# Kernel optimization log

Hardware: AMD Instinct MI355X
Metric: run time of the kernel (lower is better)

## Reference

```python
import jax, jax.numpy as jnp
import numpy as np

LN_EPS = 1e-5


def setup_inputs() -> dict:
    key = jax.random.key(0)
    k1, k2, k3 = jax.random.split(key, 3)
    B, E, IN, OUT = 16384, 8, 1024, 1024
    w_bound = (6.0 / (IN * OUT)) ** 0.5
    x = jax.random.normal(k1, (B, IN), dtype=jnp.float32)
    coef = jax.random.uniform(k2, (B, E), dtype=jnp.float32)
    w = jax.random.uniform(k3, (E, OUT, IN), dtype=jnp.float32,
                           minval=-w_bound, maxval=w_bound)
    b = jnp.zeros((E, OUT), dtype=jnp.float32)
    gamma = jnp.ones((OUT,), dtype=jnp.float32)
    beta = jnp.zeros((OUT,), dtype=jnp.float32)
    return {"x": x, "coef": coef, "w": w, "b": b, "gamma": gamma, "beta": beta}


def reference(x, coef, w, b, gamma, beta):
    # Soft-MoE linear: algebraically identical to the torch einsum chain
    #   w_b = einsum('be,ejk->bjk'); y = einsum('bk,bjk->bj') + einsum('be,ek->bk')
    # Reordered to avoid materializing [B,out,in]:
    #   per-expert projections [B,E,out], then coef-weighted combine.
    y = jnp.einsum('bk,ejk->bej', x, w)          # [B, E, out]
    y = jnp.einsum('be,bej->bj', coef, y)        # [B, out]
    y = y + coef @ b                              # [B, out]
    # LayerNorm(out_channels)
    mu = jnp.mean(y, axis=-1, keepdims=True)
    var = jnp.mean(jnp.square(y - mu), axis=-1, keepdims=True)
    y = (y - mu) * jax.lax.rsqrt(var + LN_EPS) * gamma + beta
    # GELU (torch nn.GELU default = exact erf form)
    y = jax.nn.gelu(y, approximate=False)
    return y
```

## Files before the change

### kernel.cpp

```cpp
#include <hip/hip_runtime.h>
#include <hip/hip_bf16.h>


typedef __attribute__((ext_vector_type(8))) short bf16x8;
typedef __attribute__((ext_vector_type(4))) float f32x4;

__device__ __forceinline__ unsigned short f2bf_rn(float f) {
    union { float f; unsigned u; } v; v.f = f;
    unsigned r = v.u + 0x7FFFu + ((v.u >> 16) & 1u);
    return (unsigned short)(r >> 16);
}
__device__ __forceinline__ float bf2f(unsigned short h) {
    union { unsigned u; float f; } v; v.u = ((unsigned)h) << 16; return v.f;
}

__global__ __launch_bounds__(256) void split_f32_bf16(
        const float* __restrict__ in, unsigned short* __restrict__ hi,
        unsigned short* __restrict__ lo, int n4) {
    int i = blockIdx.x * blockDim.x + threadIdx.x;
    const int stride = gridDim.x * blockDim.x;
    for (; i < n4; i += stride) {
        float4 v = ((const float4*)in)[i];
        ushort4 h, l;
        h.x = f2bf_rn(v.x); l.x = f2bf_rn(v.x - bf2f(h.x));
        h.y = f2bf_rn(v.y); l.y = f2bf_rn(v.y - bf2f(h.y));
        h.z = f2bf_rn(v.z); l.z = f2bf_rn(v.z - bf2f(h.z));
        h.w = f2bf_rn(v.w); l.w = f2bf_rn(v.w - bf2f(h.w));
        ((ushort4*)hi)[i] = h;
        ((ushort4*)lo)[i] = l;
    }
}

#define BM 256
#define BN 128
#define BK 32
#define NT 512

#define GLD(gp, lp) __builtin_amdgcn_global_load_lds( \
    (const __attribute__((address_space(1))) void*)(gp), \
    (__attribute__((address_space(3))) void*)(lp), 16, 0, 0)

__global__ __launch_bounds__(NT, 2) void gemm_moe(
        const unsigned short* __restrict__ xh, const unsigned short* __restrict__ xl,
        const unsigned short* __restrict__ wh, const unsigned short* __restrict__ wl,
        const float* __restrict__ coef, float* __restrict__ y) {
    __shared__ unsigned short As_h[BM * BK];
    __shared__ unsigned short As_l[BM * BK];
    __shared__ unsigned short Bs_h[BN * BK];
    __shared__ unsigned short Bs_l[BN * BK];

    const int bid = blockIdx.x;
    const int nb = bid & 7;
    const int mb = bid >> 3;
    const int m0 = mb * BM, n0 = nb * BN;
    const int t = threadIdx.x;
    const int lane = t & 63;
    const int wid = t >> 6;
    const int wm = wid >> 1, wn = wid & 1;
    const int lr = lane & 15, kg = lane >> 4;

    const int ar = t >> 2;
    const int acs = (t & 3) ^ (ar & 3);
    const unsigned short* agh = xh + (size_t)(m0 + ar) * 1024 + acs * 8;
    const unsigned short* agl = xl + (size_t)(m0 + ar) * 1024 + acs * 8;
    const int br = t >> 2;
    const int bcs = (t & 3) ^ (br & 3);
    const size_t bofs = (size_t)(n0 + br) * 1024 + bcs * 8;

    int aoff[4], boff[4];
#pragma unroll
    for (int i = 0; i < 4; ++i) {
        int row = wm * 64 + i * 16 + lr;
        aoff[i] = row * BK + ((kg ^ (lr & 3)) * 8);
    }
#pragma unroll
    for (int j = 0; j < 4; ++j) {
        int row = wn * 64 + j * 16 + lr;
        boff[j] = row * BK + ((kg ^ (lr & 3)) * 8);
    }

    f32x4 acc_t[4][4] = {};

    for (int e = 0; e < 8; ++e) {
        f32x4 acc[4][4] = {};
        const unsigned short* wh_e = wh + (size_t)e * 1048576 + bofs;
        const unsigned short* wl_e = wl + (size_t)e * 1048576 + bofs;
#pragma unroll 1
        for (int kt = 0; kt < 1024 / BK; ++kt) {
            const int k = kt * BK;
            __syncthreads();
            GLD(agh + k,          As_h + t * 8);
            GLD(agh + 131072 + k, As_h + 4096 + t * 8);
            GLD(agl + k,          As_l + t * 8);
            GLD(agl + 131072 + k, As_l + 4096 + t * 8);
            GLD(wh_e + k,         Bs_h + t * 8);
            GLD(wl_e + k,         Bs_l + t * 8);
            __syncthreads();

            bf16x8 ah[4], al[4], bh[4], bl[4];
#pragma unroll
            for (int i = 0; i < 4; ++i) {
                ah[i] = *(const bf16x8*)(As_h + aoff[i]);
                al[i] = *(const bf16x8*)(As_l + aoff[i]);
            }
#pragma unroll
            for (int j = 0; j < 4; ++j) {
                bh[j] = *(const bf16x8*)(Bs_h + boff[j]);
                bl[j] = *(const bf16x8*)(Bs_l + boff[j]);
            }
#pragma unroll
            for (int i = 0; i < 4; ++i)
#pragma unroll
                for (int j = 0; j < 4; ++j) {
                    acc[i][j] = __builtin_amdgcn_mfma_f32_16x16x32_bf16(
                        ah[i], bh[j], acc[i][j], 0, 0, 0);
                    acc[i][j] = __builtin_amdgcn_mfma_f32_16x16x32_bf16(
                        ah[i], bl[j], acc[i][j], 0, 0, 0);
                    acc[i][j] = __builtin_amdgcn_mfma_f32_16x16x32_bf16(
                        al[i], bh[j], acc[i][j], 0, 0, 0);
                }
        }
#pragma unroll
        for (int i = 0; i < 4; ++i) {
            const int mrow = m0 + wm * 64 + i * 16 + kg * 4;
#pragma unroll
            for (int r = 0; r < 4; ++r) {
                const float c = coef[(size_t)(mrow + r) * 8 + e];
#pragma unroll
                for (int j = 0; j < 4; ++j)
                    acc_t[i][j][r] += c * acc[i][j][r];
            }
        }
    }

#pragma unroll
    for (int i = 0; i < 4; ++i) {
        const int m = m0 + wm * 64 + i * 16 + kg * 4;
#pragma unroll
        for (int j = 0; j < 4; ++j) {
            const int n = n0 + wn * 64 + j * 16 + lr;
#pragma unroll
            for (int r = 0; r < 4; ++r)
                y[(size_t)(m + r) * 1024 + n] = acc_t[i][j][r];
        }
    }
}

__global__ __launch_bounds__(256) void ln_gelu(
        const float* __restrict__ y, const float* __restrict__ coef,
        const float* __restrict__ bexp, const float* __restrict__ gamma,
        const float* __restrict__ beta, float* __restrict__ out) {
    const int b = blockIdx.x;
    const int t = threadIdx.x;
    float4 v = ((const float4*)(y + (size_t)b * 1024))[t];

    float c[8];
#pragma unroll
    for (int e = 0; e < 8; ++e) c[e] = coef[(size_t)b * 8 + e];
    float bx = 0.f, by = 0.f, bz = 0.f, bw = 0.f;
#pragma unroll
    for (int e = 0; e < 8; ++e) {
        float4 w4 = ((const float4*)(bexp + (size_t)e * 1024))[t];
        bx += c[e] * w4.x; by += c[e] * w4.y;
        bz += c[e] * w4.z; bw += c[e] * w4.w;
    }
    v.x += bx; v.y += by; v.z += bz; v.w += bw;

    float s = v.x + v.y + v.z + v.w;
    float s2 = v.x * v.x + v.y * v.y + v.z * v.z + v.w * v.w;
#pragma unroll
    for (int off = 32; off >= 1; off >>= 1) {
        s  += __shfl_xor(s,  off);
        s2 += __shfl_xor(s2, off);
    }
    __shared__ float red[8];
    const int lane = t & 63, w = t >> 6;
    if (lane == 0) { red[w] = s; red[4 + w] = s2; }
    __syncthreads();
    s  = red[0] + red[1] + red[2] + red[3];
    s2 = red[4] + red[5] + red[6] + red[7];

    const float mu = s * (1.0f / 1024.0f);
    const float var = s2 * (1.0f / 1024.0f) - mu * mu;
    const float rstd = rsqrtf(var + 1e-5f);
    float4 g = ((const float4*)gamma)[t];
    float4 be = ((const float4*)beta)[t];
    float4 o;
    {
        float yy = (v.x - mu) * rstd * g.x + be.x;
        o.x = 0.5f * yy * (1.0f + erff(yy * 0.70710678118654752f));
        yy = (v.y - mu) * rstd * g.y + be.y;
        o.y = 0.5f * yy * (1.0f + erff(yy * 0.70710678118654752f));
        yy = (v.z - mu) * rstd * g.z + be.z;
        o.z = 0.5f * yy * (1.0f + erff(yy * 0.70710678118654752f));
        yy = (v.w - mu) * rstd * g.w + be.w;
        o.w = 0.5f * yy * (1.0f + erff(yy * 0.70710678118654752f));
    }
    ((float4*)(out + (size_t)b * 1024))[t] = o;
}

extern "C" void kernel_launch(void* const* d_in, const int* in_sizes, int n_in,
                              void* d_out, int out_size, void* d_ws, size_t ws_size,
                              hipStream_t stream) {
    (void)in_sizes; (void)n_in; (void)out_size; (void)ws_size;
    const float* x     = (const float*)d_in[0];
    const float* coef  = (const float*)d_in[1];
    const float* w     = (const float*)d_in[2];
    const float* bexp  = (const float*)d_in[3];
    const float* gamma = (const float*)d_in[4];
    const float* beta  = (const float*)d_in[5];
    float* out = (float*)d_out;

    unsigned short* xh = (unsigned short*)d_ws;
    unsigned short* xl = xh + 16777216;
    unsigned short* wh = xl + 16777216;
    unsigned short* wl = wh + 8388608;
    float* ymid = (float*)(wl + 8388608);

    split_f32_bf16<<<2048, 256, 0, stream>>>(x, xh, xl, 16777216 / 4);
    split_f32_bf16<<<1024, 256, 0, stream>>>(w, wh, wl, 8388608 / 4);
    gemm_moe<<<512, NT, 0, stream>>>(xh, xl, wh, wl, coef, ymid);
    ln_gelu<<<16384, 256, 0, stream>>>(ymid, coef, bexp, gamma, beta, out);
}
```

Before: 1.084 ms.

## Triple-buffer GEMM K-loop with 32x32 MFMA and LDS-staged coefficients

Restructures the MoE GEMM main loop into one flattened loop over expert×K tiles with a three-stage LDS ring buffer. Global-to-LDS loads are issued two stages ahead and fenced with explicit vmcnt waits and a single barrier per iteration. The MFMA shape moves from 16x16x32 to 32x32x16, and the coefficients are cached in shared memory with MFMA priority raised around the compute. The intent is to hide load latency and cut the per-tile double-barrier stall, at the cost of three times the LDS (about 152KB per block), which may limit occupancy to one block per CU.

```diff
diff --git a/kernel.cpp b/kernel.cpp
--- a/kernel.cpp
+++ b/kernel.cpp
@@ -3,7 +3,7 @@
 
 
 typedef __attribute__((ext_vector_type(8))) short bf16x8;
-typedef __attribute__((ext_vector_type(4))) float f32x4;
+typedef __attribute__((ext_vector_type(16))) float f32x16;
 
 __device__ __forceinline__ unsigned short f2bf_rn(float f) {
     union { float f; unsigned u; } v; v.f = f;
@@ -31,119 +31,135 @@
     }
 }
 
-#define BM 256
-#define BN 128
-#define BK 32
-#define NT 512
+#define BUF_USH 24576
 
 #define GLD(gp, lp) __builtin_amdgcn_global_load_lds( \
     (const __attribute__((address_space(1))) void*)(gp), \
     (__attribute__((address_space(3))) void*)(lp), 16, 0, 0)
 
-__global__ __launch_bounds__(NT, 2) void gemm_moe(
+__global__ __launch_bounds__(512, 2) void gemm_moe(
         const unsigned short* __restrict__ xh, const unsigned short* __restrict__ xl,
         const unsigned short* __restrict__ wh, const unsigned short* __restrict__ wl,
         const float* __restrict__ coef, float* __restrict__ y) {
-    __shared__ unsigned short As_h[BM * BK];
-    __shared__ unsigned short As_l[BM * BK];
-    __shared__ unsigned short Bs_h[BN * BK];
-    __shared__ unsigned short Bs_l[BN * BK];
+    __shared__ unsigned short S[3 * BUF_USH];
+    __shared__ float coef_s[2048];
 
     const int bid = blockIdx.x;
     const int nb = bid & 7;
     const int mb = bid >> 3;
-    const int m0 = mb * BM, n0 = nb * BN;
+    const int m0 = mb * 256, n0 = nb * 128;
     const int t = threadIdx.x;
     const int lane = t & 63;
     const int wid = t >> 6;
     const int wm = wid >> 1, wn = wid & 1;
-    const int lr = lane & 15, kg = lane >> 4;
+    const int lr = lane & 31, hi = lane >> 5;
+
+    ((float4*)coef_s)[t] = ((const float4*)(coef + (size_t)m0 * 8))[t];
+    __syncthreads();
 
     const int ar = t >> 2;
-    const int acs = (t & 3) ^ (ar & 3);
+    const int acs = (t & 3) ^ ((ar >> 1) & 3);
     const unsigned short* agh = xh + (size_t)(m0 + ar) * 1024 + acs * 8;
     const unsigned short* agl = xl + (size_t)(m0 + ar) * 1024 + acs * 8;
-    const int br = t >> 2;
-    const int bcs = (t & 3) ^ (br & 3);
-    const size_t bofs = (size_t)(n0 + br) * 1024 + bcs * 8;
-
-    int aoff[4], boff[4];
-#pragma unroll
-    for (int i = 0; i < 4; ++i) {
-        int row = wm * 64 + i * 16 + lr;
-        aoff[i] = row * BK + ((kg ^ (lr & 3)) * 8);
-    }
-#pragma unroll
-    for (int j = 0; j < 4; ++j) {
-        int row = wn * 64 + j * 16 + lr;
-        boff[j] = row * BK + ((kg ^ (lr & 3)) * 8);
-    }
-
-    f32x4 acc_t[4][4] = {};
-
-    for (int e = 0; e < 8; ++e) {
-        f32x4 acc[4][4] = {};
-        const unsigned short* wh_e = wh + (size_t)e * 1048576 + bofs;
-        const unsigned short* wl_e = wl + (size_t)e * 1048576 + bofs;
+    const size_t bofs = (size_t)(n0 + ar) * 1024 + acs * 8;
+    const unsigned short* wgh = wh + bofs;
+    const unsigned short* wgl = wl + bofs;
+
+    int aoff[2][2], boff[2][2];
+#pragma unroll
+    for (int i = 0; i < 2; ++i)
+#pragma unroll
+        for (int s = 0; s < 2; ++s) {
+            const int slot = ((s << 1) + hi) ^ ((lr >> 1) & 3);
+            aoff[i][s] = (wm * 64 + i * 32 + lr) * 32 + slot * 8;
+            boff[i][s] = (wn * 64 + i * 32 + lr) * 32 + slot * 8;
+        }
+
+    f32x16 acc[2][2] = {};
+    f32x16 acc_t[2][2] = {};
+
+    auto STAGE = [&](int kt2, int bufi) {
+        unsigned short* bp = S + bufi * BUF_USH;
+        const size_t eo = (size_t)(kt2 >> 5) << 20;
+        const int ko = (kt2 & 31) << 5;
+        GLD(agh + ko,           bp + t * 8);
+        GLD(agh + 131072 + ko,  bp + 4096 + t * 8);
+        GLD(agl + ko,           bp + 8192 + t * 8);
+        GLD(agl + 131072 + ko,  bp + 12288 + t * 8);
+        GLD(wgh + eo + ko,      bp + 16384 + t * 8);
+        GLD(wgl + eo + ko,      bp + 20480 + t * 8);
+    };
+
+    STAGE(0, 0);
+    STAGE(1, 1);
+    asm volatile("s_waitcnt vmcnt(6)" ::: "memory");
+    __builtin_amdgcn_s_barrier();
+
+    int cur = 0;
 #pragma unroll 1
-        for (int kt = 0; kt < 1024 / BK; ++kt) {
-            const int k = kt * BK;
-            __syncthreads();
-            GLD(agh + k,          As_h + t * 8);
-            GLD(agh + 131072 + k, As_h + 4096 + t * 8);
-            GLD(agl + k,          As_l + t * 8);
-            GLD(agl + 131072 + k, As_l + 4096 + t * 8);
-            GLD(wh_e + k,         Bs_h + t * 8);
-            GLD(wl_e + k,         Bs_l + t * 8);
-            __syncthreads();
-
-            bf16x8 ah[4], al[4], bh[4], bl[4];
-#pragma unroll
-            for (int i = 0; i < 4; ++i) {
-                ah[i] = *(const bf16x8*)(As_h + aoff[i]);
-                al[i] = *(const bf16x8*)(As_l + aoff[i]);
+    for (int kt = 0; kt < 256; ++kt) {
+        const unsigned short* bp = S + cur * BUF_USH;
+        bf16x8 ah[2][2], al[2][2], bh2[2][2], bl2[2][2];
+#pragma unroll
+        for (int i = 0; i < 2; ++i)
+#pragma unroll
+            for (int s = 0; s < 2; ++s) {
+                ah[i][s]  = *(const bf16x8*)(bp + aoff[i][s]);
+                al[i][s]  = *(const bf16x8*)(bp + 8192 + aoff[i][s]);
+                bh2[i][s] = *(const bf16x8*)(bp + 16384 + boff[i][s]);
+                bl2[i][s] = *(const bf16x8*)(bp + 20480 + boff[i][s]);
             }
-#pragma unroll
-            for (int j = 0; j < 4; ++j) {
-                bh[j] = *(const bf16x8*)(Bs_h + boff[j]);
-                bl[j] = *(const bf16x8*)(Bs_l + boff[j]);
+        if (kt < 254) {
+            int stg = cur + 2; if (stg >= 3) stg -= 3;
+            STAGE(kt + 2, stg);
+        }
+
+        __builtin_amdgcn_s_setprio(1);
+#pragma unroll
+        for (int s = 0; s < 2; ++s)
+#pragma unroll
+            for (int i = 0; i < 2; ++i)
+#pragma unroll
+                for (int j = 0; j < 2; ++j) {
+                    acc[i][j] = __builtin_amdgcn_mfma_f32_32x32x16_bf16(
+                        ah[i][s], bh2[j][s], acc[i][j], 0, 0, 0);
+                    acc[i][j] = __builtin_amdgcn_mfma_f32_32x32x16_bf16(
+                        ah[i][s], bl2[j][s], acc[i][j], 0, 0, 0);
+                    acc[i][j] = __builtin_amdgcn_mfma_f32_32x32x16_bf16(
+                        al[i][s], bh2[j][s], acc[i][j], 0, 0, 0);
+                }
+        __builtin_amdgcn_s_setprio(0);
+
+        if ((kt & 31) == 31) {
+            const int e = kt >> 5;
+#pragma unroll
+            for (int i = 0; i < 2; ++i)
+#pragma unroll
+                for (int r = 0; r < 16; ++r) {
+                    const int row = wm * 64 + i * 32 + (r & 3) + 8 * (r >> 2) + 4 * hi;
+                    const float c = coef_s[row * 8 + e];
+                    acc_t[i][0][r] += c * acc[i][0][r]; acc[i][0][r] = 0.f;
+                    acc_t[i][1][r] += c * acc[i][1][r]; acc[i][1][r] = 0.f;
+                }
+        }
+
+        if (kt < 254) asm volatile("s_waitcnt vmcnt(6)" ::: "memory");
+        else          asm volatile("s_waitcnt vmcnt(0)" ::: "memory");
+        __builtin_amdgcn_s_barrier();
+        cur = (cur == 2) ? 0 : cur + 1;
+    }
+
+#pragma unroll
+    for (int i = 0; i < 2; ++i)
+#pragma unroll
+        for (int j = 0; j < 2; ++j) {
+            const int n = n0 + wn * 64 + j * 32 + lr;
+#pragma unroll
+            for (int r = 0; r < 16; ++r) {
+                const int m = m0 + wm * 64 + i * 32 + (r & 3) + 8 * (r >> 2) + 4 * hi;
+                y[(size_t)m * 1024 + n] = acc_t[i][j][r];
             }
-#pragma unroll
-            for (int i = 0; i < 4; ++i)
-#pragma unroll
-                for (int j = 0; j < 4; ++j) {
-                    acc[i][j] = __builtin_amdgcn_mfma_f32_16x16x32_bf16(
-                        ah[i], bh[j], acc[i][j], 0, 0, 0);
-                    acc[i][j] = __builtin_amdgcn_mfma_f32_16x16x32_bf16(
-                        ah[i], bl[j], acc[i][j], 0, 0, 0);
-                    acc[i][j] = __builtin_amdgcn_mfma_f32_16x16x32_bf16(
-                        al[i], bh[j], acc[i][j], 0, 0, 0);
-                }
-        }
-#pragma unroll
-        for (int i = 0; i < 4; ++i) {
-            const int mrow = m0 + wm * 64 + i * 16 + kg * 4;
-#pragma unroll
-            for (int r = 0; r < 4; ++r) {
-                const float c = coef[(size_t)(mrow + r) * 8 + e];
-#pragma unroll
-                for (int j = 0; j < 4; ++j)
-                    acc_t[i][j][r] += c * acc[i][j][r];
-            }
-        }
-    }
-
-#pragma unroll
-    for (int i = 0; i < 4; ++i) {
-        const int m = m0 + wm * 64 + i * 16 + kg * 4;
-#pragma unroll
-        for (int j = 0; j < 4; ++j) {
-            const int n = n0 + wn * 64 + j * 16 + lr;
-#pragma unroll
-            for (int r = 0; r < 4; ++r)
-                y[(size_t)(m + r) * 1024 + n] = acc_t[i][j][r];
-        }
-    }
+        }
 }
 
 __global__ __launch_bounds__(256) void ln_gelu(
@@ -219,6 +235,6 @@
 
     split_f32_bf16<<<2048, 256, 0, stream>>>(x, xh, xl, 16777216 / 4);
     split_f32_bf16<<<1024, 256, 0, stream>>>(w, wh, wl, 8388608 / 4);
-    gemm_moe<<<512, NT, 0, stream>>>(xh, xl, wh, wl, coef, ymid);
+    gemm_moe<<<512, 512, 0, stream>>>(xh, xl, wh, wl, coef, ymid);
     ln_gelu<<<16384, 256, 0, stream>>>(ymid, coef, bexp, gamma, beta, out);
 }
```

Result: faster. 969.9 us (-10.6%).
